# Kernel optimization log

Hardware: AMD Instinct MI355X
Metric: run time of the kernel (lower is better)

## Reference

```python
import jax, jax.numpy as jnp
import numpy as np

B, T, I, H = 256, 512, 300, 128


def setup_inputs() -> dict:
    key = jax.random.key(0)
    ks = jax.random.split(key, 7)
    s_ih = 1.0 / np.sqrt(H)
    return {
        "x": jax.random.normal(ks[0], (B, T, I), dtype=jnp.float32),
        # PyTorch LSTM params, gate order i,f,g,o stacked along first axis
        "W_ih": jax.random.uniform(ks[1], (4 * H, I), minval=-s_ih, maxval=s_ih, dtype=jnp.float32),
        "W_hh": jax.random.uniform(ks[2], (4 * H, H), minval=-s_ih, maxval=s_ih, dtype=jnp.float32),
        "b_ih": jax.random.uniform(ks[3], (4 * H,), minval=-s_ih, maxval=s_ih, dtype=jnp.float32),
        "b_hh": jax.random.uniform(ks[4], (4 * H,), minval=-s_ih, maxval=s_ih, dtype=jnp.float32),
        "fc_w": jax.random.uniform(ks[5], (1, H), minval=-s_ih, maxval=s_ih, dtype=jnp.float32),
        "fc_b": jax.random.uniform(ks[6], (1,), minval=-s_ih, maxval=s_ih, dtype=jnp.float32),
    }


def _lstm_last_h(x, W_ih, W_hh, b_ih, b_hh):
    # Precompute input contributions for all timesteps at once: [B,T,4H]
    xg = jnp.einsum("bti,gi->btg", x, W_ih) + b_ih + b_hh
    xg = jnp.transpose(xg, (1, 0, 2))  # [T,B,4H] for scan

    def step(carry, xg_t):
        h, c = carry
        gates = xg_t + h @ W_hh.T  # [B,4H]
        i, f, g, o = jnp.split(gates, 4, axis=-1)
        i = jax.nn.sigmoid(i)
        f = jax.nn.sigmoid(f)
        g = jnp.tanh(g)
        o = jax.nn.sigmoid(o)
        c = f * c + i * g
        h = o * jnp.tanh(c)
        return (h, c), None

    h0 = jnp.zeros((x.shape[0], W_hh.shape[1]), dtype=x.dtype)
    (h_last, _), _ = jax.lax.scan(step, (h0, h0), xg)
    return h_last  # [B,H]


def reference(x, W_ih, W_hh, b_ih, b_hh, fc_w, fc_b):
    h_last = _lstm_last_h(x, W_ih, W_hh, b_ih, b_hh)
    return h_last @ fc_w.T + fc_b  # [B,1]
```

## Files before the change

### kernel.cpp

```cpp
#include <hip/hip_runtime.h>
#include <cstdint>
#include <cstddef>

#define Bb   256
#define Tt   512
#define Ii   300
#define Hh   128
#define G4   512
#define KP   320
#define Mm   (Bb*Tt)

typedef _Float16 h2v   __attribute__((ext_vector_type(2)));
typedef _Float16 half8 __attribute__((ext_vector_type(8)));
typedef float    f32x4 __attribute__((ext_vector_type(4)));

static __device__ __forceinline__ h2v as_h2(unsigned int u){ union{unsigned int u; h2v h;} c; c.u=u; return c.h; }
static __device__ __forceinline__ unsigned int as_u32(h2v h){ union{unsigned int u; h2v h;} c; c.h=h; return c.u; }

#if __has_builtin(__builtin_amdgcn_fdot2)
#define FDOT2(a,b,c) __builtin_amdgcn_fdot2((a),(b),(c),false)
#else
static __device__ __forceinline__ float FDOT2(h2v a, h2v b, float c){
  return c + (float)a[0]*(float)b[0] + (float)a[1]*(float)b[1];
}
#endif

__global__ __launch_bounds__(256) void conv_x(const float* __restrict__ x, unsigned int* __restrict__ x16){
  int idx = blockIdx.x*256 + threadIdx.x;
  int r   = idx / 160;
  int kk2 = idx - r*160;
  int kk  = kk2*2;
  const float* xr = x + (size_t)r*Ii;
  float v0 = (kk   < Ii) ? xr[kk]   : 0.f;
  float v1 = (kk+1 < Ii) ? xr[kk+1] : 0.f;
  h2v h; h[0] = (_Float16)v0; h[1] = (_Float16)v1;
  x16[idx] = as_u32(h);
}

__global__ __launch_bounds__(256) void conv_small(const float* __restrict__ Wih, const float* __restrict__ Whh,
      const float* __restrict__ bih, const float* __restrict__ bhh,
      unsigned int* __restrict__ W16, unsigned int* __restrict__ Whh2, float* __restrict__ bias){
  int idx = blockIdx.x*256 + threadIdx.x;
  if (idx < G4*160){
    int r = idx/160, kk2 = idx - r*160, kk = kk2*2;
    const float* wr = Wih + (size_t)r*Ii;
    float v0 = (kk   < Ii) ? wr[kk]   : 0.f;
    float v1 = (kk+1 < Ii) ? wr[kk+1] : 0.f;
    h2v h; h[0]=(_Float16)v0; h[1]=(_Float16)v1;
    W16[idx] = as_u32(h);
  } else if (idx < G4*160 + G4*64){
    int t = idx - G4*160; int j = t>>6, kk = t&63;
    float v0 = Whh[j*Hh + kk*2], v1 = Whh[j*Hh + kk*2 + 1];
    h2v h; h[0]=(_Float16)v0; h[1]=(_Float16)v1;
    Whh2[t] = as_u32(h);
  } else if (idx < G4*160 + G4*64 + G4){
    int d = idx - (G4*160 + G4*64);
    bias[d] = bih[d] + bhh[d];
  }
}

__global__ __launch_bounds__(256,2) void gemm16(const _Float16* __restrict__ A, const _Float16* __restrict__ Bm,
       const float* __restrict__ bias, float* __restrict__ C){
  __shared__ _Float16 As[128][32];
  __shared__ _Float16 Bs[128][32];
  int tid = threadIdx.x;
  int w = tid>>6, lane = tid&63;
  int bm = blockIdx.x*128, bn = blockIdx.y*128;
  f32x4 acc[2][8];
  #pragma unroll
  for (int i=0;i<2;i++)
    #pragma unroll
    for (int j=0;j<8;j++) acc[i][j] = (f32x4){0.f,0.f,0.f,0.f};

  int srow = tid>>1, scol = (tid&1)*16;
  const uint4* ga = (const uint4*)(A  + (size_t)(bm+srow)*KP + scol);
  const uint4* gb = (const uint4*)(Bm + (size_t)(bn+srow)*KP + scol);

  int q = lane>>4, mr = lane&15;
  int m0 = w*32;

  for (int kt=0; kt<KP/32; ++kt){
    __syncthreads();
    uint4 va0 = ga[0], va1 = ga[1];
    uint4 vb0 = gb[0], vb1 = gb[1];
    *(uint4*)&As[srow][scol]   = va0; *(uint4*)&As[srow][scol+8] = va1;
    *(uint4*)&Bs[srow][scol]   = vb0; *(uint4*)&Bs[srow][scol+8] = vb1;
    ga += 4; gb += 4;
    __syncthreads();
    half8 af0 = *(const half8*)&As[m0 + mr][q*8];
    half8 af1 = *(const half8*)&As[m0 + 16 + mr][q*8];
    #pragma unroll
    for (int j=0;j<8;j++){
      half8 bf = *(const half8*)&Bs[j*16 + mr][q*8];
      acc[0][j] = __builtin_amdgcn_mfma_f32_16x16x32_f16(af0, bf, acc[0][j], 0,0,0);
      acc[1][j] = __builtin_amdgcn_mfma_f32_16x16x32_f16(af1, bf, acc[1][j], 0,0,0);
    }
  }
  #pragma unroll
  for (int j=0;j<8;j++){
    int gc = bn + j*16 + mr;
    float bv = bias[gc];
    #pragma unroll
    for (int i=0;i<2;i++){
      int gr0 = bm + w*32 + i*16 + q*4;
      #pragma unroll
      for (int reg=0; reg<4; ++reg)
        C[(size_t)(gr0+reg)*G4 + gc] = acc[i][j][reg] + bv;
    }
  }
}

__global__ __launch_bounds__(512,2) void lstm_rec(const float* __restrict__ xg, const unsigned int* __restrict__ Whh2,
     const float* __restrict__ fcw, const float* __restrict__ fcb, float* __restrict__ out){
  int tid = threadIdx.x;
  int b = blockIdx.x;
  int d = tid & 127, g = tid >> 7;
  h2v w[64];
  #pragma unroll
  for (int kk=0; kk<64; ++kk) w[kk] = as_h2(Whh2[tid*64 + kk]);

  __shared__ __align__(16) unsigned short hsh[128];
  __shared__ __align__(16) float gsh[512];
  __shared__ float red[128];
  if (tid < 128) hsh[tid] = 0;
  float creg = 0.f, hreg = 0.f;
  const float* xrow = xg + (size_t)b * (Tt*G4);
  float xc = xrow[tid];
  __syncthreads();

  for (int t=0; t<Tt; ++t){
    float xn = 0.f;
    if (t < Tt-1) xn = xrow[(size_t)(t+1)*G4 + tid];
    float a0 = xc, a1 = 0.f;
    const uint4* hv = (const uint4*)hsh;
    #pragma unroll
    for (int kq=0; kq<8; ++kq){
      uint4 hq0 = hv[kq*2], hq1 = hv[kq*2+1];
      a0 = FDOT2(as_h2(hq0.x), w[kq*8+0], a0); a1 = FDOT2(as_h2(hq0.y), w[kq*8+1], a1);
      a0 = FDOT2(as_h2(hq0.z), w[kq*8+2], a0); a1 = FDOT2(as_h2(hq0.w), w[kq*8+3], a1);
      a0 = FDOT2(as_h2(hq1.x), w[kq*8+4], a0); a1 = FDOT2(as_h2(hq1.y), w[kq*8+5], a1);
      a0 = FDOT2(as_h2(hq1.z), w[kq*8+6], a0); a1 = FDOT2(as_h2(hq1.w), w[kq*8+7], a1);
    }
    float a = a0 + a1;
    float act;
    if (g == 2){ float e = __expf(2.f*a); act = 1.f - 2.f/(e+1.f); }
    else       { act = 1.f/(1.f+__expf(-a)); }
    gsh[d*4+g] = act;
    __syncthreads();
    float4 gv = *(const float4*)&gsh[d*4];
    creg = gv.y*creg + gv.x*gv.z;
    float ec = __expf(2.f*creg); float tc = 1.f - 2.f/(ec+1.f);
    hreg = gv.w*tc;
    if (g == 0){
      union{ _Float16 f; unsigned short s; } cv; cv.f = (_Float16)hreg;
      hsh[d] = cv.s;
    }
    __syncthreads();
    xc = xn;
  }

  if (tid < 128) red[tid] = hreg * fcw[tid];
  __syncthreads();
  #pragma unroll
  for (int s=64; s>=1; s>>=1){
    if (tid < s) red[tid] += red[tid+s];
    __syncthreads();
  }
  if (tid == 0) out[b] = red[0] + fcb[0];
}

extern "C" void kernel_launch(void* const* d_in, const int* in_sizes, int n_in,
                              void* d_out, int out_size, void* d_ws, size_t ws_size,
                              hipStream_t stream){
  const float* x   = (const float*)d_in[0];
  const float* Wih = (const float*)d_in[1];
  const float* Whh = (const float*)d_in[2];
  const float* bih = (const float*)d_in[3];
  const float* bhh = (const float*)d_in[4];
  const float* fcw = (const float*)d_in[5];
  const float* fcb = (const float*)d_in[6];
  float* out = (float*)d_out;
  char* ws = (char*)d_ws;

  unsigned int* x16   = (unsigned int*)(ws);
  unsigned int* W16   = (unsigned int*)(ws + 83886080);
  unsigned int* Whh2w = (unsigned int*)(ws + 84213760);
  float*        bias  = (float*)      (ws + 84344832);
  float*        xg    = (float*)      (ws + 84346880);

  hipLaunchKernelGGL(conv_x,     dim3(81920),  dim3(256), 0, stream, x, x16);
  hipLaunchKernelGGL(conv_small, dim3(450),    dim3(256), 0, stream, Wih, Whh, bih, bhh, W16, Whh2w, bias);
  hipLaunchKernelGGL(gemm16,     dim3(1024,4), dim3(256), 0, stream,
                     (const _Float16*)x16, (const _Float16*)W16, bias, xg);
  hipLaunchKernelGGL(lstm_rec,   dim3(256),    dim3(512), 0, stream, xg, Whh2w, fcw, fcb, out);
}
```

Measured before the change: 660.5 us.

## Interleave gate columns so LSTM gates exchange via shuffles, not shared memory

New measurement: 638.9 us. 3.3% less time.

```diff
diff --git a/kernel.cpp b/kernel.cpp
--- a/kernel.cpp
+++ b/kernel.cpp
@@ -42,20 +42,23 @@
       unsigned int* __restrict__ W16, unsigned int* __restrict__ Whh2, float* __restrict__ bias){
   int idx = blockIdx.x*256 + threadIdx.x;
   if (idx < G4*160){
-    int r = idx/160, kk2 = idx - r*160, kk = kk2*2;
-    const float* wr = Wih + (size_t)r*Ii;
+    int pr = idx/160, kk2 = idx - pr*160, kk = kk2*2;
+    int gc = (pr&3)*128 + (pr>>2);
+    const float* wr = Wih + (size_t)gc*Ii;
     float v0 = (kk   < Ii) ? wr[kk]   : 0.f;
     float v1 = (kk+1 < Ii) ? wr[kk+1] : 0.f;
     h2v h; h[0]=(_Float16)v0; h[1]=(_Float16)v1;
     W16[idx] = as_u32(h);
   } else if (idx < G4*160 + G4*64){
-    int t = idx - G4*160; int j = t>>6, kk = t&63;
-    float v0 = Whh[j*Hh + kk*2], v1 = Whh[j*Hh + kk*2 + 1];
+    int t = idx - G4*160; int pr = t>>6, kk = t&63;
+    int gc = (pr&3)*128 + (pr>>2);
+    float v0 = Whh[gc*Hh + kk*2], v1 = Whh[gc*Hh + kk*2 + 1];
     h2v h; h[0]=(_Float16)v0; h[1]=(_Float16)v1;
     Whh2[t] = as_u32(h);
   } else if (idx < G4*160 + G4*64 + G4){
-    int d = idx - (G4*160 + G4*64);
-    bias[d] = bih[d] + bhh[d];
+    int pr = idx - (G4*160 + G4*64);
+    int gc = (pr&3)*128 + (pr>>2);
+    bias[pr] = bih[gc] + bhh[gc];
   }
 }
 
@@ -110,60 +113,69 @@
   }
 }
 
-__global__ __launch_bounds__(512,2) void lstm_rec(const float* __restrict__ xg, const unsigned int* __restrict__ Whh2,
+__global__ __launch_bounds__(512,1) void lstm_rec(const float* __restrict__ xg, const unsigned int* __restrict__ Whh2,
      const float* __restrict__ fcw, const float* __restrict__ fcb, float* __restrict__ out){
   int tid = threadIdx.x;
   int b = blockIdx.x;
-  int d = tid & 127, g = tid >> 7;
+  int d = tid >> 2, g = tid & 3;
   h2v w[64];
   #pragma unroll
   for (int kk=0; kk<64; ++kk) w[kk] = as_h2(Whh2[tid*64 + kk]);
 
-  __shared__ __align__(16) unsigned short hsh[128];
-  __shared__ __align__(16) float gsh[512];
+  __shared__ __align__(16) unsigned short hsh[2][128];
   __shared__ float red[128];
-  if (tid < 128) hsh[tid] = 0;
+  if (tid < 128) hsh[0][tid] = 0;
   float creg = 0.f, hreg = 0.f;
   const float* xrow = xg + (size_t)b * (Tt*G4);
   float xc = xrow[tid];
+  int b0 = g & 1;
+  int b1 = (g >> 1) & 1;
+  float km = (g == 2) ? 2.f : 1.f;
   __syncthreads();
 
   for (int t=0; t<Tt; ++t){
     float xn = 0.f;
     if (t < Tt-1) xn = xrow[(size_t)(t+1)*G4 + tid];
-    float a0 = xc, a1 = 0.f;
-    const uint4* hv = (const uint4*)hsh;
+    const uint4* hv = (const uint4*)hsh[t & 1];
+    float a0 = xc, a1 = 0.f, a2 = 0.f, a3 = 0.f;
     #pragma unroll
     for (int kq=0; kq<8; ++kq){
       uint4 hq0 = hv[kq*2], hq1 = hv[kq*2+1];
       a0 = FDOT2(as_h2(hq0.x), w[kq*8+0], a0); a1 = FDOT2(as_h2(hq0.y), w[kq*8+1], a1);
-      a0 = FDOT2(as_h2(hq0.z), w[kq*8+2], a0); a1 = FDOT2(as_h2(hq0.w), w[kq*8+3], a1);
+      a2 = FDOT2(as_h2(hq0.z), w[kq*8+2], a2); a3 = FDOT2(as_h2(hq0.w), w[kq*8+3], a3);
       a0 = FDOT2(as_h2(hq1.x), w[kq*8+4], a0); a1 = FDOT2(as_h2(hq1.y), w[kq*8+5], a1);
-      a0 = FDOT2(as_h2(hq1.z), w[kq*8+6], a0); a1 = FDOT2(as_h2(hq1.w), w[kq*8+7], a1);
-    }
-    float a = a0 + a1;
-    float act;
-    if (g == 2){ float e = __expf(2.f*a); act = 1.f - 2.f/(e+1.f); }
-    else       { act = 1.f/(1.f+__expf(-a)); }
-    gsh[d*4+g] = act;
-    __syncthreads();
-    float4 gv = *(const float4*)&gsh[d*4];
-    creg = gv.y*creg + gv.x*gv.z;
+      a2 = FDOT2(as_h2(hq1.z), w[kq*8+6], a2); a3 = FDOT2(as_h2(hq1.w), w[kq*8+7], a3);
+    }
+    float a = (a0 + a1) + (a2 + a3);
+    float s  = 1.f/(1.f + __expf(-km*a));
+    float act = (g == 2) ? (2.f*s - 1.f) : s;
+    float u1 = __shfl_xor(act, 1);
+    float u2 = __shfl_xor(act, 2);
+    float u3 = __shfl_xor(act, 3);
+    float pl = b0 ? u1  : act;
+    float ph = b0 ? u3  : u2;
+    float ql = b0 ? act : u1;
+    float qh = b0 ? u2  : u3;
+    float i_ = b1 ? ph : pl;
+    float f_ = b1 ? qh : ql;
+    float g_ = b1 ? pl : ph;
+    float o_ = b1 ? ql : qh;
+    creg = f_*creg + i_*g_;
     float ec = __expf(2.f*creg); float tc = 1.f - 2.f/(ec+1.f);
-    hreg = gv.w*tc;
+    hreg = o_*tc;
     if (g == 0){
       union{ _Float16 f; unsigned short s; } cv; cv.f = (_Float16)hreg;
-      hsh[d] = cv.s;
+      hsh[(t+1) & 1][d] = cv.s;
     }
     __syncthreads();
     xc = xn;
   }
 
-  if (tid < 128) red[tid] = hreg * fcw[tid];
+  if (g == 0) red[d] = hreg * fcw[d];
   __syncthreads();
   #pragma unroll
-  for (int s=64; s>=1; s>>=1){
-    if (tid < s) red[tid] += red[tid+s];
+  for (int s2=64; s2>=1; s2>>=1){
+    if (tid < s2) red[tid] += red[tid+s2];
     __syncthreads();
   }
   if (tid == 0) out[b] = red[0] + fcb[0];
```
